# Kernel optimization log

Measured on AMD Instinct MI355X. Metric: run time of the kernel, lower is better.

The kernel has to match this reference:

```python
import jax, jax.numpy as jnp
import numpy as np

DT = 0.5
NE, NIN = 400, 784
# excitatory LIF
THRESH_E, OFFSET, VRESET_E, EREST_E, REFRAC_E, TAU_MEM_E = -52.0, 20.0, -65.0, -65.0, 5.0, 100.0
# inhibitory LIF
THRESH_I, VRESET_I, EREST_I, REFRAC_I, TAU_MEM_I = -40.0, -45.0, -60.0, 2.0, 10.0
# synapses
TAU_SYN_E, TAU_SYN_I = 1.0, 2.0
E_EI, E_IE, E_EE = 0.0, -100.0, 0.0
# STDP
TC_P1, TC_P2, TC_PRE = 20.0, 40.0, 20.0
NU_PRE, NU_POST, WMAX = 0.0001, 0.01, 1.0
THETA0 = 20.0


def lif_step(mem, rc, I, thresh, v_reset, erest, tau, refrac):
    # conductance-based LIF with refractory period (inferred LIFei semantics)
    active = rc <= 0.0
    mem = jnp.where(active, mem + (erest - mem + I) * (DT / tau), mem)
    rc = jnp.maximum(rc - DT, 0.0)
    spike = (active & (mem > thresh)).astype(mem.dtype)
    fired = spike > 0.0
    mem = jnp.where(fired, v_reset, mem)
    rc = jnp.where(fired, refrac, rc)
    return mem, rc, spike


def setup_inputs() -> dict:
    key = jax.random.key(0)
    k1, k2 = jax.random.split(key)
    x = jax.random.uniform(k1, (50, 512, NIN), dtype=jnp.float32)  # Poisson-rate encoded frames
    W_ine = (jax.random.uniform(k2, (NE, NIN), dtype=jnp.float32) + 0.01) * 0.3  # create_ine
    W_ei = jnp.eye(NE, dtype=jnp.float32) * 10.4                                  # create_ei
    W_ie = (jnp.ones((NE, NE), jnp.float32) - jnp.eye(NE, dtype=jnp.float32)) * 17.0  # create_ie
    return {"x": x, "W_ine": W_ine, "W_ei": W_ei, "W_ie": W_ie}


def reference(x, W_ine, W_ei, W_ie):
    T, B, _ = x.shape
    z_e = jnp.zeros((B, NE), x.dtype)

    def step(carry, xt_t):
        xt, t = xt_t
        (W, g_ine, g_ei, g_ie, Iie, mem_e, rc_e, mem_i, rc_i,
         theta, tr_pre, tp1, tp2) = carry
        # normweight: rows sum to 78.4
        W = W / (jnp.sum(W, axis=1, keepdims=True) / 78.4)
        # input -> e synapse (STDP-plastic)
        dg_ine = xt @ W.T                         # (B, NE)
        I_ine = g_ine * (E_EE - mem_e)            # g=0 at t=0 -> I=0 (matches None init)
        g_ine = g_ine + (dg_ine - g_ine) * (DT / TAU_SYN_E)
        # excitatory LIF with adaptive threshold
        thr_e = THRESH_E - OFFSET + theta
        mem_e, rc_e, spike_e = lif_step(mem_e, rc_e, I_ine + Iie, thr_e,
                                        VRESET_E, EREST_E, TAU_MEM_E, REFRAC_E)
        # e -> i synapse
        dg_ei = spike_e @ W_ei.T
        I_ei = g_ei * (E_EI - mem_i)
        g_ei = g_ei + (dg_ei - g_ei) * (DT / TAU_SYN_E)
        # inhibitory LIF
        mem_i, rc_i, spike_i = lif_step(mem_i, rc_i, I_ei, THRESH_I,
                                        VRESET_I, EREST_I, TAU_MEM_I, REFRAC_I)
        # i -> e synapse (current fed into NEXT step's lif_e)
        dg_ie = spike_i @ W_ie.T
        Iie = g_ie * (E_IE - mem_e)
        g_ie = g_ie + (dg_ie - g_ie) * (DT / TAU_SYN_I)
        # threshold homeostasis
        theta = theta * (1.0 - DT / 1e7) + 0.05 * spike_e
        # pre trace: first call copies x, later decay then set to 1 where x>0.9
        tr_pre_upd = jnp.where(xt > 0.9, 1.0, tr_pre * (1.0 - DT / TC_PRE))
        tr_pre = jnp.where(t == 0, xt, tr_pre_upd)
        # post traces: return decayed value, then set to 1 where spike
        ret1 = tp1 * (1.0 - DT / TC_P1)
        ret2 = tp2 * (1.0 - DT / TC_P2)
        fired = spike_e > 0.9
        tp1 = jnp.where(fired, 1.0, ret1)
        tp2 = jnp.where(fired, 1.0, ret2)
        # STDP: autograd.grad of dg=x@W^T w.r.t. W with grad_outputs G is G^T @ x
        dw = (NU_PRE * jnp.einsum('be,bi->ei', ret1, xt)
              + NU_POST * jnp.einsum('be,bi->ei', spike_e * ret2, tr_pre))
        W = jnp.clip(W + dw, 0.0, WMAX)
        new_carry = (W, g_ine, g_ei, g_ie, Iie, mem_e, rc_e, mem_i, rc_i,
                     theta, tr_pre, tp1, tp2)
        return new_carry, spike_e

    carry0 = (W_ine,
              z_e, z_e, z_e,                      # g_ine, g_ei, g_ie
              z_e,                                # Iie
              jnp.full((B, NE), EREST_E, x.dtype), z_e,   # mem_e, rc_e
              jnp.full((B, NE), EREST_I, x.dtype), z_e,   # mem_i, rc_i
              jnp.full((B, NE), THETA0, x.dtype),         # theta
              jnp.zeros((B, NIN), x.dtype),               # trace_pre
              z_e, z_e)                                   # trace_post1/2
    _, spikes = jax.lax.scan(step, carry0, (x, jnp.arange(T)))
    return spikes  # (T, B, NE)
```

## Files before the change

kernel.cpp:

```cpp
#include <hip/hip_runtime.h>

#define NE 400
#define NIN 784
#define BB 512
#define TT 50

#define KC1 7
#define KCH1 112
#define KC2 8
#define KCH2 128

constexpr float C_KE     = (float)(0.5 / 100.0);
constexpr float C_KI     = (float)(0.5 / 10.0);
constexpr float C_GSE    = 0.5f;
constexpr float C_GSI    = 0.25f;
constexpr float C_DECTH  = (float)(1.0 - 0.5 / 1e7);
constexpr float C_DEC1   = (float)(1.0 - 0.5 / 20.0);
constexpr float C_DEC2   = (float)(1.0 - 0.5 / 40.0);
constexpr float C_DECPRE = (float)(1.0 - 0.5 / 20.0);
constexpr float C_NUPRE  = (float)0.0001;
constexpr float C_NUPOST = 0.01f;

__global__ void k_init(float* g_ine, float* g_ei, float* g_ie, float* Iie,
                       float* mem_e, float* rc_e, float* mem_i, float* rc_i,
                       float* theta, float* tp1, float* tp2) {
    int i = blockIdx.x * blockDim.x + threadIdx.x;
    if (i < BB * NE) {
        g_ine[i] = 0.f; g_ei[i] = 0.f; g_ie[i] = 0.f; Iie[i] = 0.f;
        mem_e[i] = -65.0f; rc_e[i] = 0.f;
        mem_i[i] = -60.0f; rc_i[i] = 0.f;
        theta[i] = 20.0f; tp1[i] = 0.f; tp2[i] = 0.f;
    }
}

__global__ __launch_bounds__(256) void k_rowsum0(const float* __restrict__ W,
                                                 float* __restrict__ d) {
    int e = blockIdx.x, tid = threadIdx.x;
    __shared__ float red[256];
    float s = 0.f;
    if (tid < 196) {
        float4 w = *(const float4*)&W[e * NIN + tid * 4];
        s = w.x + w.y + w.z + w.w;
    }
    red[tid] = s;
    __syncthreads();
    for (int off = 128; off > 0; off >>= 1) {
        if (tid < off) red[tid] += red[tid + off];
        __syncthreads();
    }
    if (tid == 0) d[e] = red[0] / 78.4f;
}

__global__ __launch_bounds__(256) void k_g1(const float* __restrict__ x,
                                            const float* __restrict__ W,
                                            float* __restrict__ dgp) {
    __shared__ float sA[16][68];
    __shared__ float sB[16][132];
    const int lid = threadIdx.x;
    const int tx = lid & 15, ty = lid >> 4;
    const int e0 = blockIdx.x * 128, b0 = blockIdx.y * 64;
    const int kb = blockIdx.z * KCH1;
    const int sr = lid >> 2;
    const int sj = (lid & 3) * 4;
    const float4 z4 = make_float4(0.f, 0.f, 0.f, 0.f);

    float acc[4][2][4];
#pragma unroll
    for (int p = 0; p < 4; p++)
#pragma unroll
        for (int h = 0; h < 2; h++)
#pragma unroll
            for (int q = 0; q < 4; q++) acc[p][h][q] = 0.f;

    float4 xv, wv0, wv1;
    auto ld = [&](int kt) {
        int k0 = kb + kt * 16;
        xv = *(const float4*)&x[(b0 + sr) * NIN + k0 + sj];
        int e1 = e0 + sr, e2 = e0 + 64 + sr;
        wv0 = (e1 < NE) ? *(const float4*)&W[e1 * NIN + k0 + sj] : z4;
        wv1 = (e2 < NE) ? *(const float4*)&W[e2 * NIN + k0 + sj] : z4;
    };

    ld(0);
    for (int kt = 0; kt < KCH1 / 16; kt++) {
        sA[sj + 0][sr] = xv.x; sA[sj + 1][sr] = xv.y;
        sA[sj + 2][sr] = xv.z; sA[sj + 3][sr] = xv.w;
        sB[sj + 0][sr] = wv0.x; sB[sj + 1][sr] = wv0.y;
        sB[sj + 2][sr] = wv0.z; sB[sj + 3][sr] = wv0.w;
        sB[sj + 0][64 + sr] = wv1.x; sB[sj + 1][64 + sr] = wv1.y;
        sB[sj + 2][64 + sr] = wv1.z; sB[sj + 3][64 + sr] = wv1.w;
        __syncthreads();
        if (kt < KCH1 / 16 - 1) ld(kt + 1);
#pragma unroll
        for (int k = 0; k < 16; k++) {
            float4 av = *(const float4*)&sA[k][ty * 4];
            float4 b0v = *(const float4*)&sB[k][tx * 4];
            float4 b1v = *(const float4*)&sB[k][64 + tx * 4];
            float a[4] = {av.x, av.y, av.z, av.w};
            float bq0[4] = {b0v.x, b0v.y, b0v.z, b0v.w};
            float bq1[4] = {b1v.x, b1v.y, b1v.z, b1v.w};
#pragma unroll
            for (int p = 0; p < 4; p++)
#pragma unroll
                for (int q = 0; q < 4; q++) {
                    acc[p][0][q] += a[p] * bq0[q];
                    acc[p][1][q] += a[p] * bq1[q];
                }
        }
        __syncthreads();
    }
    float* basep = dgp + (size_t)blockIdx.z * BB * NE;
    int c1 = e0 + tx * 4, c2 = e0 + 64 + tx * 4;
#pragma unroll
    for (int p = 0; p < 4; p++) {
        int row = b0 + ty * 4 + p;
        if (c1 < NE)
            *(float4*)&basep[row * NE + c1] =
                make_float4(acc[p][0][0], acc[p][0][1], acc[p][0][2], acc[p][0][3]);
        if (c2 < NE)
            *(float4*)&basep[row * NE + c2] =
                make_float4(acc[p][1][0], acc[p][1][1], acc[p][1][2], acc[p][1][3]);
    }
}

__global__ __launch_bounds__(512) void k_mid(const float* __restrict__ dgp,
                                             const float* __restrict__ d,
                                             const float* __restrict__ xt,
                                             float* __restrict__ tr, int t,
                                             float* g_ine, float* g_ei, float* g_ie,
                                             float* Iie, float* mem_e, float* rc_e,
                                             float* mem_i, float* rc_i, float* theta,
                                             float* tp1, float* tp2,
                                             float* __restrict__ A1s,
                                             float* __restrict__ A2s,
                                             float* __restrict__ out_t) {
    if (blockIdx.x >= BB) {
        int base = (blockIdx.x - BB) * 2048 + threadIdx.x * 4;
        float4 xv = *(const float4*)&xt[base];
        float4 o;
        if (t == 0) {
            o = xv;
        } else {
            float4 tv = *(const float4*)&tr[base];
            o.x = (xv.x > 0.9f) ? 1.f : tv.x * C_DECPRE;
            o.y = (xv.y > 0.9f) ? 1.f : tv.y * C_DECPRE;
            o.z = (xv.z > 0.9f) ? 1.f : tv.z * C_DECPRE;
            o.w = (xv.w > 0.9f) ? 1.f : tv.w * C_DECPRE;
        }
        *(float4*)&tr[base] = o;
        return;
    }
    int b = blockIdx.x;
    int e = threadIdx.x;
    __shared__ float red[8];
    int idx = b * NE + e;

    float spk_i = 0.f, spk_e = 0.f;
    float g1 = 0.f, me = 0.f, re = 0.f, th = 0.f, g2 = 0.f, mi = 0.f, ri = 0.f;

    if (e < NE) {
        float dg = 0.f;
#pragma unroll
        for (int c = 0; c < KC1; c++) dg += dgp[(size_t)c * BB * NE + idx];
        dg = dg / d[e];
        g1 = g_ine[idx]; me = mem_e[idx]; re = rc_e[idx];
        th = theta[idx];
        float Ii = Iie[idx];
        float I_in = g1 * (0.0f - me);
        g1 = g1 + (dg - g1) * C_GSE;
        bool act = (re <= 0.0f);
        float I = I_in + Ii;
        if (act) me = me + ((-65.0f - me) + I) * C_KE;
        re = fmaxf(re - 0.5f, 0.0f);
        float thr = -72.0f + th;
        spk_e = (act && (me > thr)) ? 1.0f : 0.0f;
        if (spk_e > 0.0f) { me = -65.0f; re = 5.0f; }
        float dgei = spk_e * 10.4f;
        g2 = g_ei[idx]; mi = mem_i[idx]; ri = rc_i[idx];
        float I_ei = g2 * (0.0f - mi);
        g2 = g2 + (dgei - g2) * C_GSE;
        bool ai = (ri <= 0.0f);
        if (ai) mi = mi + ((-60.0f - mi) + I_ei) * C_KI;
        ri = fmaxf(ri - 0.5f, 0.0f);
        spk_i = (ai && (mi > -40.0f)) ? 1.0f : 0.0f;
        if (spk_i > 0.0f) { mi = -45.0f; ri = 2.0f; }
    }
    float v = spk_i;
#pragma unroll
    for (int o = 32; o > 0; o >>= 1) v += __shfl_down(v, o, 64);
    if ((e & 63) == 0) red[e >> 6] = v;
    __syncthreads();
    float S = ((red[0] + red[1]) + (red[2] + red[3])) +
              ((red[4] + red[5]) + (red[6] + red[7]));
    if (e < NE) {
        float dgie = 17.0f * (S - spk_i);
        float g3 = g_ie[idx];
        float Iie_new = g3 * (-100.0f - me);
        g3 = g3 + (dgie - g3) * C_GSI;
        float th2 = th * C_DECTH + 0.05f * spk_e;
        float r1 = tp1[idx] * C_DEC1;
        float r2 = tp2[idx] * C_DEC2;
        bool fired = spk_e > 0.9f;
        A1s[idx] = C_NUPRE * r1;
        A2s[idx] = C_NUPOST * (spk_e * r2);
        tp1[idx] = fired ? 1.0f : r1;
        tp2[idx] = fired ? 1.0f : r2;
        g_ine[idx] = g1; g_ei[idx] = g2; g_ie[idx] = g3; Iie[idx] = Iie_new;
        mem_e[idx] = me; rc_e[idx] = re; mem_i[idx] = mi; rc_i[idx] = ri;
        theta[idx] = th2;
        out_t[idx] = spk_e;
    }
}

__global__ __launch_bounds__(256) void k_g2(const float* __restrict__ A1s,
                                            const float* __restrict__ A2s,
                                            const float* __restrict__ x,
                                            const float* __restrict__ tr,
                                            float* __restrict__ part) {
    __shared__ float sA[16][68];
    __shared__ float sB[16][132];
    const int lid = threadIdx.x;
    const int tx = lid & 15, ty = lid >> 4;
    const int e0 = blockIdx.x * 64, i0 = blockIdx.y * 128;
    const int kb = blockIdx.z * KCH2;
    const int kr = lid >> 4;
    const int jc = (lid & 15) * 4;
    const float4 z4 = make_float4(0.f, 0.f, 0.f, 0.f);

    float acc[4][2][4];
#pragma unroll
    for (int p = 0; p < 4; p++)
#pragma unroll
        for (int h = 0; h < 2; h++)
#pragma unroll
            for (int q = 0; q < 4; q++) acc[p][h][q] = 0.f;

    float4 av_, bv0_, bv1_;
    auto ld = [&](int kt) {
        int gb = kb + kt * 16 + kr;
        int ec = e0 + jc;
        if (ec < NE)
            av_ = (gb < BB) ? *(const float4*)&A1s[gb * NE + ec]
                            : *(const float4*)&A2s[(gb - BB) * NE + ec];
        else av_ = z4;
        const float* src; int rb;
        if (gb < BB) { src = x; rb = gb; } else { src = tr; rb = gb - BB; }
        int c1 = i0 + jc, c2 = i0 + 64 + jc;
        bv0_ = (c1 < NIN) ? *(const float4*)&src[rb * NIN + c1] : z4;
        bv1_ = (c2 < NIN) ? *(const float4*)&src[rb * NIN + c2] : z4;
    };

    ld(0);
    for (int kt = 0; kt < KCH2 / 16; kt++) {
        *(float4*)&sA[kr][jc] = av_;
        *(float4*)&sB[kr][jc] = bv0_;
        *(float4*)&sB[kr][64 + jc] = bv1_;
        __syncthreads();
        if (kt < KCH2 / 16 - 1) ld(kt + 1);
#pragma unroll
        for (int k = 0; k < 16; k++) {
            float4 av = *(const float4*)&sA[k][ty * 4];
            float4 b0v = *(const float4*)&sB[k][tx * 4];
            float4 b1v = *(const float4*)&sB[k][64 + tx * 4];
            float a[4] = {av.x, av.y, av.z, av.w};
            float bq0[4] = {b0v.x, b0v.y, b0v.z, b0v.w};
            float bq1[4] = {b1v.x, b1v.y, b1v.z, b1v.w};
#pragma unroll
            for (int p = 0; p < 4; p++)
#pragma unroll
                for (int q = 0; q < 4; q++) {
                    acc[p][0][q] += a[p] * bq0[q];
                    acc[p][1][q] += a[p] * bq1[q];
                }
        }
        __syncthreads();
    }
    float* basep = part + (size_t)blockIdx.z * NE * NIN;
    int c1 = i0 + tx * 4, c2 = i0 + 64 + tx * 4;
#pragma unroll
    for (int p = 0; p < 4; p++) {
        int row = e0 + ty * 4 + p;
        if (row < NE) {
            if (c1 < NIN)
                *(float4*)&basep[row * NIN + c1] =
                    make_float4(acc[p][0][0], acc[p][0][1], acc[p][0][2], acc[p][0][3]);
            if (c2 < NIN)
                *(float4*)&basep[row * NIN + c2] =
                    make_float4(acc[p][1][0], acc[p][1][1], acc[p][1][2], acc[p][1][3]);
        }
    }
}

__global__ __launch_bounds__(256) void k_wup(float* __restrict__ W,
                                             const float* __restrict__ part,
                                             float* __restrict__ d) {
    int e = blockIdx.x, tid = threadIdx.x;
    __shared__ float red[256];
    float dv = d[e];
    float s = 0.f;
    if (tid < 196) {
        int off = e * NIN + tid * 4;
        float4 w = *(const float4*)&W[off];
        float4 acc = make_float4(w.x / dv, w.y / dv, w.z / dv, w.w / dv);
#pragma unroll
        for (int c = 0; c < KC2; c++) {
            float4 p = *(const float4*)&part[(size_t)c * NE * NIN + off];
            acc.x += p.x; acc.y += p.y; acc.z += p.z; acc.w += p.w;
        }
        acc.x = fminf(fmaxf(acc.x, 0.f), 1.f);
        acc.y = fminf(fmaxf(acc.y, 0.f), 1.f);
        acc.z = fminf(fmaxf(acc.z, 0.f), 1.f);
        acc.w = fminf(fmaxf(acc.w, 0.f), 1.f);
        *(float4*)&W[off] = acc;
        s = acc.x + acc.y + acc.z + acc.w;
    }
    red[tid] = s;
    __syncthreads();
    for (int off = 128; off > 0; off >>= 1) {
        if (tid < off) red[tid] += red[tid + off];
        __syncthreads();
    }
    if (tid == 0) d[e] = red[0] / 78.4f;
}

extern "C" void kernel_launch(void* const* d_in, const int* in_sizes, int n_in,
                              void* d_out, int out_size, void* d_ws, size_t ws_size,
                              hipStream_t stream) {
    const float* x     = (const float*)d_in[0];
    const float* W_ine = (const float*)d_in[1];

    float* p = (float*)d_ws;
    float* W_cur = p; p += NE * NIN;
    float* dbuf  = p; p += NE;
    float* dgp   = p; p += (size_t)KC1 * BB * NE;
    float* part  = p; p += (size_t)KC2 * NE * NIN;
    float* A1s   = p; p += BB * NE;
    float* A2s   = p; p += BB * NE;
    float* g_ine = p; p += BB * NE;
    float* g_ei  = p; p += BB * NE;
    float* g_ie  = p; p += BB * NE;
    float* Iie   = p; p += BB * NE;
    float* mem_e = p; p += BB * NE;
    float* rc_e  = p; p += BB * NE;
    float* mem_i = p; p += BB * NE;
    float* rc_i  = p; p += BB * NE;
    float* theta = p; p += BB * NE;
    float* tp1   = p; p += BB * NE;
    float* tp2   = p; p += BB * NE;
    float* tr    = p; p += BB * NIN;

    hipMemcpyAsync(W_cur, W_ine, (size_t)NE * NIN * sizeof(float),
                   hipMemcpyDeviceToDevice, stream);
    k_init<<<(BB * NE + 255) / 256, 256, 0, stream>>>(g_ine, g_ei, g_ie, Iie, mem_e,
                                                      rc_e, mem_i, rc_i, theta, tp1, tp2);
    k_rowsum0<<<NE, 256, 0, stream>>>(W_cur, dbuf);

    for (int t = 0; t < TT; t++) {
        const float* xt = x + (size_t)t * BB * NIN;
        float* out_t = (float*)d_out + (size_t)t * BB * NE;
        k_g1<<<dim3(4, 8, KC1), 256, 0, stream>>>(xt, W_cur, dgp);
        k_mid<<<BB + 196, 512, 0, stream>>>(dgp, dbuf, xt, tr, t, g_ine, g_ei, g_ie,
                                            Iie, mem_e, rc_e, mem_i, rc_i, theta,
                                            tp1, tp2, A1s, A2s, out_t);
        if (t < TT - 1) {
            k_g2<<<dim3(7, 7, KC2), 256, 0, stream>>>(A1s, A2s, xt, tr, part);
            k_wup<<<NE, 256, 0, stream>>>(W_cur, part, dbuf);
        }
    }
}
```

Before: 2.232 ms.

## Double split-K chunks for both GEMMs and move trace update into weight-update kernel

Doubles the split-K factor for the forward GEMM (14 chunks of 56) and the STDP GEMM (16 chunks of 64) to launch more blocks. The k_g1 smem tile shrinks to 8-deep k steps with a new load mapping. The presynaptic trace update moves out of k_mid into k_wup, which now prepares next step's trace, and into a new k_pre for t=0. More partial buffers must be summed in k_mid and k_wup, raising partial-sum memory traffic.

Result: faster. 2.098 ms (-6.0%).

```diff
diff --git a/kernel.cpp b/kernel.cpp
--- a/kernel.cpp
+++ b/kernel.cpp
@@ -5,10 +5,11 @@
 #define BB 512
 #define TT 50
 
-#define KC1 7
-#define KCH1 112
-#define KC2 8
-#define KCH2 128
+#define KC1 14
+#define KCH1 56
+#define KT1 8
+#define KC2 16
+#define KCH2 64
 
 constexpr float C_KE     = (float)(0.5 / 100.0);
 constexpr float C_KI     = (float)(0.5 / 10.0);
@@ -33,13 +34,20 @@
     }
 }
 
-__global__ __launch_bounds__(256) void k_rowsum0(const float* __restrict__ W,
-                                                 float* __restrict__ d) {
-    int e = blockIdx.x, tid = threadIdx.x;
+__global__ __launch_bounds__(256) void k_pre(const float* __restrict__ W,
+                                             float* __restrict__ d,
+                                             const float* __restrict__ x0,
+                                             float* __restrict__ tr) {
+    int bid = blockIdx.x, tid = threadIdx.x;
+    if (bid >= NE) {
+        int base = (bid - NE) * 2048 + tid * 4;
+        *(float4*)&tr[base] = *(const float4*)&x0[base];
+        return;
+    }
     __shared__ float red[256];
     float s = 0.f;
     if (tid < 196) {
-        float4 w = *(const float4*)&W[e * NIN + tid * 4];
+        float4 w = *(const float4*)&W[bid * NIN + tid * 4];
         s = w.x + w.y + w.z + w.w;
     }
     red[tid] = s;
@@ -48,20 +56,21 @@
         if (tid < off) red[tid] += red[tid + off];
         __syncthreads();
     }
-    if (tid == 0) d[e] = red[0] / 78.4f;
+    if (tid == 0) d[bid] = red[0] / 78.4f;
 }
 
 __global__ __launch_bounds__(256) void k_g1(const float* __restrict__ x,
                                             const float* __restrict__ W,
                                             float* __restrict__ dgp) {
-    __shared__ float sA[16][68];
-    __shared__ float sB[16][132];
+    __shared__ float sA[KT1][68];
+    __shared__ float sB[KT1][132];
     const int lid = threadIdx.x;
     const int tx = lid & 15, ty = lid >> 4;
     const int e0 = blockIdx.x * 128, b0 = blockIdx.y * 64;
     const int kb = blockIdx.z * KCH1;
-    const int sr = lid >> 2;
-    const int sj = (lid & 3) * 4;
+    const int xr = lid >> 2, xc = (lid & 3) * 2;
+    const int wr = lid >> 1, wc = (lid & 1) * 4;
+    const bool wv_ok = (e0 + wr) < NE;
     const float4 z4 = make_float4(0.f, 0.f, 0.f, 0.f);
 
     float acc[4][2][4];
@@ -72,27 +81,23 @@
 #pragma unroll
             for (int q = 0; q < 4; q++) acc[p][h][q] = 0.f;
 
-    float4 xv, wv0, wv1;
+    float2 xv;
+    float4 wv;
     auto ld = [&](int kt) {
-        int k0 = kb + kt * 16;
-        xv = *(const float4*)&x[(b0 + sr) * NIN + k0 + sj];
-        int e1 = e0 + sr, e2 = e0 + 64 + sr;
-        wv0 = (e1 < NE) ? *(const float4*)&W[e1 * NIN + k0 + sj] : z4;
-        wv1 = (e2 < NE) ? *(const float4*)&W[e2 * NIN + k0 + sj] : z4;
+        int k0 = kb + kt * KT1;
+        xv = *(const float2*)&x[(b0 + xr) * NIN + k0 + xc];
+        wv = wv_ok ? *(const float4*)&W[(e0 + wr) * NIN + k0 + wc] : z4;
     };
 
     ld(0);
-    for (int kt = 0; kt < KCH1 / 16; kt++) {
-        sA[sj + 0][sr] = xv.x; sA[sj + 1][sr] = xv.y;
-        sA[sj + 2][sr] = xv.z; sA[sj + 3][sr] = xv.w;
-        sB[sj + 0][sr] = wv0.x; sB[sj + 1][sr] = wv0.y;
-        sB[sj + 2][sr] = wv0.z; sB[sj + 3][sr] = wv0.w;
-        sB[sj + 0][64 + sr] = wv1.x; sB[sj + 1][64 + sr] = wv1.y;
-        sB[sj + 2][64 + sr] = wv1.z; sB[sj + 3][64 + sr] = wv1.w;
-        __syncthreads();
-        if (kt < KCH1 / 16 - 1) ld(kt + 1);
-#pragma unroll
-        for (int k = 0; k < 16; k++) {
+    for (int kt = 0; kt < KCH1 / KT1; kt++) {
+        sA[xc + 0][xr] = xv.x; sA[xc + 1][xr] = xv.y;
+        sB[wc + 0][wr] = wv.x; sB[wc + 1][wr] = wv.y;
+        sB[wc + 2][wr] = wv.z; sB[wc + 3][wr] = wv.w;
+        __syncthreads();
+        if (kt < KCH1 / KT1 - 1) ld(kt + 1);
+#pragma unroll
+        for (int k = 0; k < KT1; k++) {
             float4 av = *(const float4*)&sA[k][ty * 4];
             float4 b0v = *(const float4*)&sB[k][tx * 4];
             float4 b1v = *(const float4*)&sB[k][64 + tx * 4];
@@ -125,8 +130,6 @@
 
 __global__ __launch_bounds__(512) void k_mid(const float* __restrict__ dgp,
                                              const float* __restrict__ d,
-                                             const float* __restrict__ xt,
-                                             float* __restrict__ tr, int t,
                                              float* g_ine, float* g_ei, float* g_ie,
                                              float* Iie, float* mem_e, float* rc_e,
                                              float* mem_i, float* rc_i, float* theta,
@@ -134,22 +137,6 @@
                                              float* __restrict__ A1s,
                                              float* __restrict__ A2s,
                                              float* __restrict__ out_t) {
-    if (blockIdx.x >= BB) {
-        int base = (blockIdx.x - BB) * 2048 + threadIdx.x * 4;
-        float4 xv = *(const float4*)&xt[base];
-        float4 o;
-        if (t == 0) {
-            o = xv;
-        } else {
-            float4 tv = *(const float4*)&tr[base];
-            o.x = (xv.x > 0.9f) ? 1.f : tv.x * C_DECPRE;
-            o.y = (xv.y > 0.9f) ? 1.f : tv.y * C_DECPRE;
-            o.z = (xv.z > 0.9f) ? 1.f : tv.z * C_DECPRE;
-            o.w = (xv.w > 0.9f) ? 1.f : tv.w * C_DECPRE;
-        }
-        *(float4*)&tr[base] = o;
-        return;
-    }
     int b = blockIdx.x;
     int e = threadIdx.x;
     __shared__ float red[8];
@@ -293,13 +280,27 @@
 
 __global__ __launch_bounds__(256) void k_wup(float* __restrict__ W,
                                              const float* __restrict__ part,
-                                             float* __restrict__ d) {
-    int e = blockIdx.x, tid = threadIdx.x;
+                                             float* __restrict__ d,
+                                             const float* __restrict__ x1,
+                                             float* __restrict__ tr) {
+    int bid = blockIdx.x, tid = threadIdx.x;
+    if (bid >= NE) {
+        int base = (bid - NE) * 2048 + tid * 4;
+        float4 xv = *(const float4*)&x1[base];
+        float4 tv = *(const float4*)&tr[base];
+        float4 o;
+        o.x = (xv.x > 0.9f) ? 1.f : tv.x * C_DECPRE;
+        o.y = (xv.y > 0.9f) ? 1.f : tv.y * C_DECPRE;
+        o.z = (xv.z > 0.9f) ? 1.f : tv.z * C_DECPRE;
+        o.w = (xv.w > 0.9f) ? 1.f : tv.w * C_DECPRE;
+        *(float4*)&tr[base] = o;
+        return;
+    }
     __shared__ float red[256];
-    float dv = d[e];
+    float dv = d[bid];
     float s = 0.f;
     if (tid < 196) {
-        int off = e * NIN + tid * 4;
+        int off = bid * NIN + tid * 4;
         float4 w = *(const float4*)&W[off];
         float4 acc = make_float4(w.x / dv, w.y / dv, w.z / dv, w.w / dv);
 #pragma unroll
@@ -320,7 +321,7 @@
         if (tid < off) red[tid] += red[tid + off];
         __syncthreads();
     }
-    if (tid == 0) d[e] = red[0] / 78.4f;
+    if (tid == 0) d[bid] = red[0] / 78.4f;
 }
 
 extern "C" void kernel_launch(void* const* d_in, const int* in_sizes, int n_in,
@@ -353,18 +354,19 @@
                    hipMemcpyDeviceToDevice, stream);
     k_init<<<(BB * NE + 255) / 256, 256, 0, stream>>>(g_ine, g_ei, g_ie, Iie, mem_e,
                                                       rc_e, mem_i, rc_i, theta, tp1, tp2);
-    k_rowsum0<<<NE, 256, 0, stream>>>(W_cur, dbuf);
+    k_pre<<<NE + 196, 256, 0, stream>>>(W_cur, dbuf, x, tr);
 
     for (int t = 0; t < TT; t++) {
         const float* xt = x + (size_t)t * BB * NIN;
         float* out_t = (float*)d_out + (size_t)t * BB * NE;
         k_g1<<<dim3(4, 8, KC1), 256, 0, stream>>>(xt, W_cur, dgp);
-        k_mid<<<BB + 196, 512, 0, stream>>>(dgp, dbuf, xt, tr, t, g_ine, g_ei, g_ie,
-                                            Iie, mem_e, rc_e, mem_i, rc_i, theta,
-                                            tp1, tp2, A1s, A2s, out_t);
+        k_mid<<<BB, 512, 0, stream>>>(dgp, dbuf, g_ine, g_ei, g_ie,
+                                      Iie, mem_e, rc_e, mem_i, rc_i, theta,
+                                      tp1, tp2, A1s, A2s, out_t);
         if (t < TT - 1) {
             k_g2<<<dim3(7, 7, KC2), 256, 0, stream>>>(A1s, A2s, xt, tr, part);
-            k_wup<<<NE, 256, 0, stream>>>(W_cur, part, dbuf);
-        }
-    }
-}
+            k_wup<<<NE + 196, 256, 0, stream>>>(W_cur, part, dbuf,
+                                                xt + (size_t)BB * NIN, tr);
+        }
+    }
+}
```
